# Kernel optimization log

Measured on AMD Instinct MI355X. Metric: run time of the kernel, lower is better.

The kernel has to match this reference:

```python
import jax, jax.numpy as jnp
import numpy as np

EPS = 1e-5

def layer_norm(x, gamma, beta):
    mu = jnp.mean(x, axis=-1, keepdims=True)
    var = jnp.mean(jnp.square(x - mu), axis=-1, keepdims=True)
    return (x - mu) * jax.lax.rsqrt(var + EPS) * gamma + beta

def setup_inputs() -> dict:
    key = jax.random.key(0)
    ks = jax.random.split(key, 8)
    B, N, E, D, H = 8, 10000, 160000, 128, 128  # batch, nodes, edges, in_dim, dim_h
    nodes = jax.random.normal(ks[0], (B, N, D), dtype=jnp.float32)
    senders = jax.random.randint(ks[1], (E,), 0, N)
    receivers = jax.random.randint(ks[2], (E,), 0, N)
    # nn.Linear(2*in_dim, in_dim): weight [out, in], bias [out]
    Wm = jax.random.normal(ks[3], (D, 2 * D), dtype=jnp.float32) / np.sqrt(2 * D)
    bm = jnp.zeros((D,), dtype=jnp.float32)
    # nn.Linear(2*in_dim, dim_h)
    Wn = jax.random.normal(ks[4], (H, 2 * D), dtype=jnp.float32) / np.sqrt(2 * D)
    bn = jnp.zeros((H,), dtype=jnp.float32)
    g1 = jnp.ones((D,), dtype=jnp.float32)
    b1 = jnp.zeros((D,), dtype=jnp.float32)
    g2 = jnp.ones((H,), dtype=jnp.float32)
    b2 = jnp.zeros((H,), dtype=jnp.float32)
    return {"nodes": nodes, "Wm": Wm, "bm": bm, "g1": g1, "b1": b1,
            "Wn": Wn, "bn": bn, "g2": g2, "b2": b2,
            "senders": senders, "receivers": receivers}

def reference(nodes, Wm, bm, g1, b1, Wn, bn, g2, b2, senders, receivers):
    # gather endpoints: [B, E, 2*D]
    edge_in = jnp.concatenate((nodes[:, receivers], nodes[:, senders]), axis=-1)
    messages = jnp.einsum('bed,od->beo', edge_in, Wm) + bm      # [B, E, D]
    messages = layer_norm(messages, g1, b1)
    # scatter-add into inbox along node axis
    inbox = jnp.zeros_like(nodes).at[:, receivers].add(messages)  # [B, N, D]
    node_in = jnp.concatenate((nodes, inbox), axis=-1)           # [B, N, 2*D]
    out = jnp.einsum('bnd,od->bno', node_in, Wn) + bn            # [B, N, H]
    return layer_norm(out, g2, b2)
```

## Files before the change

kernel.cpp:

```cpp
#include <hip/hip_runtime.h>

#define N_NODES 10000
#define N_EDGES 160000
#define BATCH   8
#define D       128
#define TWO_D   256
#define EPS     1e-5f
#define ETILE   32
#define TPB_E   8
#define TPB_N   8

typedef _Float16 f16x8  __attribute__((ext_vector_type(8)));
typedef float    f32x16 __attribute__((ext_vector_type(16)));

__global__ void zero_kernel(float4* __restrict__ p, long long n4) {
    long long idx    = (long long)blockIdx.x * blockDim.x + threadIdx.x;
    long long stride = (long long)gridDim.x * blockDim.x;
    const float4 z = {0.f, 0.f, 0.f, 0.f};
    for (long long i = idx; i < n4; i += stride) p[i] = z;
}

__global__ void prep_w(const float* __restrict__ Wm, const float* __restrict__ Wn,
                       unsigned char* __restrict__ img) {
    int t = blockIdx.x * blockDim.x + threadIdx.x;
    if (t >= 4096) return;
    int g = t >> 7, o = t & 127;
    f16x8 vm, vn;
#pragma unroll
    for (int j = 0; j < 8; ++j) {
        vm[j] = (_Float16)Wm[o * TWO_D + 8 * g + j];
        vn[j] = (_Float16)Wn[o * TWO_D + 8 * g + j];
    }
    ((f16x8*)img)[t]           = vm;
    ((f16x8*)(img + 65536))[t] = vn;
}

__global__ void hist_kernel(const int* __restrict__ recv, int* __restrict__ counts) {
    int e = blockIdx.x * blockDim.x + threadIdx.x;
    if (e < N_EDGES) atomicAdd(&counts[recv[e]], 1);
}

__global__ __launch_bounds__(1024)
void scan_kernel(const int* __restrict__ counts, int* __restrict__ cursor) {
    __shared__ int tmp[1024];
    int t = threadIdx.x;
    int local[10];
    int s = 0;
#pragma unroll
    for (int j = 0; j < 10; ++j) {
        int idx = t * 10 + j;
        int v = (idx < N_NODES) ? counts[idx] : 0;
        local[j] = s; s += v;
    }
    tmp[t] = s; __syncthreads();
    for (int off = 1; off < 1024; off <<= 1) {
        int v = tmp[t];
        int add = (t >= off) ? tmp[t - off] : 0;
        __syncthreads();
        tmp[t] = v + add;
        __syncthreads();
    }
    int base = (t > 0) ? tmp[t - 1] : 0;
#pragma unroll
    for (int j = 0; j < 10; ++j) {
        int idx = t * 10 + j;
        if (idx < N_NODES) cursor[idx] = base + local[j];
    }
}

__global__ void scatter_kernel(const int* __restrict__ recv, int* __restrict__ cursor,
                               int* __restrict__ perm) {
    int e = blockIdx.x * blockDim.x + threadIdx.x;
    if (e < N_EDGES) {
        int p = atomicAdd(&cursor[recv[e]], 1);
        perm[p] = e;
    }
}

__global__ __launch_bounds__(256, 2)
void edge_mfma(const float* __restrict__ nodes,
               const unsigned char* __restrict__ wimg,
               const float* __restrict__ bm,
               const float* __restrict__ g1,
               const float* __restrict__ b1,
               const int*   __restrict__ senders,
               const int*   __restrict__ receivers,
               const int*   __restrict__ perm,
               float* __restrict__ inbox) {
    __shared__ __align__(16) unsigned char s_lds[33280];
    __shared__ int   s_recv[ETILE];
    __shared__ float s_mu[ETILE];
    __shared__ float s_rs[ETILE];

    const int tid    = threadIdx.x;
    const int b      = blockIdx.y;
    const int w      = tid >> 6;
    const int l      = tid & 63;
    const int lane31 = l & 31;
    const int hiG    = l >> 5;
    const int o      = w * 32 + lane31;

    f16x8 wf[16];
    {
        const f16x8* img = (const f16x8*)wimg;
#pragma unroll
        for (int ks = 0; ks < 16; ++ks)
            wf[ks] = img[(2 * ks + hiG) * 128 + o];
    }
    const float bmv = bm[o];
    const int   col  = tid & 127;
    const int   half = tid >> 7;
    const float gv = g1[col], bv = b1[col];
    float* const abase = inbox + (size_t)b * N_NODES * D + col;

    const int i  = tid & 31;
    const int q8 = tid >> 5;
    f16x8* const Xh  = (f16x8*)s_lds;
    f16x8* const Xl  = (f16x8*)(s_lds + 16384);
    float* const msg = (float*)(s_lds + 16384);

    for (int it = 0; it < TPB_E; ++it) {
        const int e0 = (blockIdx.x * TPB_E + it) * ETILE;

        {
            const int pe = perm[e0 + i];
            const int r  = (q8 < 4) ? receivers[pe] : senders[pe];
            if (q8 == 0) s_recv[i] = r;
            const float* row = nodes + ((size_t)b * N_NODES + r) * D + (q8 & 3) * 32;
#pragma unroll
            for (int j = 0; j < 4; ++j) {
                const float4 va = *(const float4*)(row + 8 * j);
                const float4 vb = *(const float4*)(row + 8 * j + 4);
                const float xs[8] = {va.x, va.y, va.z, va.w, vb.x, vb.y, vb.z, vb.w};
                f16x8 h, lo;
#pragma unroll
                for (int u = 0; u < 8; ++u) {
                    h[u]  = (_Float16)xs[u];
                    lo[u] = (_Float16)(xs[u] - (float)h[u]);
                }
                const int g = 4 * q8 + j;
                Xh[g * 32 + i] = h;
                Xl[g * 32 + i] = lo;
            }
        }
        __syncthreads();

        f32x16 acc;
#pragma unroll
        for (int r = 0; r < 16; ++r) acc[r] = 0.f;
#pragma unroll
        for (int ks = 0; ks < 16; ++ks) {
            const f16x8 ah = Xh[(2 * ks + hiG) * 32 + lane31];
            const f16x8 al = Xl[(2 * ks + hiG) * 32 + lane31];
            acc = __builtin_amdgcn_mfma_f32_32x32x16_f16(ah, wf[ks], acc, 0, 0, 0);
            acc = __builtin_amdgcn_mfma_f32_32x32x16_f16(al, wf[ks], acc, 0, 0, 0);
        }
        __syncthreads();

#pragma unroll
        for (int r = 0; r < 16; ++r) {
            const int m = (r & 3) + 8 * (r >> 2) + 4 * hiG;
            msg[m * 132 + o] = acc[r] + bmv;
        }
        __syncthreads();

        {
            const int m = tid >> 3, c0 = tid & 7;
            float s = 0.f, s2 = 0.f;
#pragma unroll
            for (int i2 = 0; i2 < 16; ++i2) {
                const float v = msg[m * 132 + c0 + 8 * i2];
                s += v; s2 += v * v;
            }
            s  += __shfl_xor(s, 1, 64);  s  += __shfl_xor(s, 2, 64);  s  += __shfl_xor(s, 4, 64);
            s2 += __shfl_xor(s2, 1, 64); s2 += __shfl_xor(s2, 2, 64); s2 += __shfl_xor(s2, 4, 64);
            if (c0 == 0) {
                const float mu  = s * (1.f / 128.f);
                const float var = s2 * (1.f / 128.f) - mu * mu;
                s_mu[m] = mu;
                s_rs[m] = rsqrtf(var + EPS);
            }
        }
        __syncthreads();

        {
            int prev = -1; float accu = 0.f;
#pragma unroll
            for (int e = 0; e < 16; ++e) {
                const int ee = half * 16 + e;
                const int r  = s_recv[ee];
                const float val = (msg[ee * 132 + col] - s_mu[ee]) * s_rs[ee] * gv + bv;
                if (r != prev) {
                    if (prev >= 0) atomicAdd(abase + (size_t)prev * D, accu);
                    prev = r; accu = val;
                } else {
                    accu += val;
                }
            }
            if (prev >= 0) atomicAdd(abase + (size_t)prev * D, accu);
        }
        __syncthreads();
    }
}

__global__ __launch_bounds__(256, 2)
void node_mfma(const float* __restrict__ nodes,
               const float* __restrict__ inbox,
               const unsigned char* __restrict__ wimg,
               const float* __restrict__ bn,
               const float* __restrict__ g2,
               const float* __restrict__ b2,
               float* __restrict__ out) {
    __shared__ __align__(16) unsigned char s_lds[33280];
    __shared__ float s_mu[ETILE];
    __shared__ float s_rs[ETILE];

    const int tid    = threadIdx.x;
    const int b      = blockIdx.y;
    const int w      = tid >> 6;
    const int l      = tid & 63;
    const int lane31 = l & 31;
    const int hiG    = l >> 5;
    const int o      = w * 32 + lane31;

    f16x8 wf[16];
    {
        const f16x8* img = (const f16x8*)wimg;
#pragma unroll
        for (int ks = 0; ks < 16; ++ks)
            wf[ks] = img[(2 * ks + hiG) * 128 + o];
    }
    const float bnv = bn[o];
    const int   col  = tid & 127;
    const int   half = tid >> 7;
    const float gv = g2[col], bv = b2[col];

    const int i  = tid & 31;
    const int q8 = tid >> 5;
    f16x8* const Xh  = (f16x8*)s_lds;
    f16x8* const Xl  = (f16x8*)(s_lds + 16384);
    float* const msg = (float*)(s_lds + 16384);

    const int NTILES = (N_NODES + ETILE - 1) / ETILE;

    for (int it = 0; it < TPB_N; ++it) {
        const int tile = blockIdx.x * TPB_N + it;
        if (tile >= NTILES) break;
        const int n0 = tile * ETILE;

        {
            int n = n0 + i;
            if (n >= N_NODES) n = N_NODES - 1;
            const float* row = (q8 < 4)
                ? (nodes + ((size_t)b * N_NODES + n) * D + (q8 & 3) * 32)
                : (inbox + ((size_t)b * N_NODES + n) * D + (q8 & 3) * 32);
#pragma unroll
            for (int j = 0; j < 4; ++j) {
                const float4 va = *(const float4*)(row + 8 * j);
                const float4 vb = *(const float4*)(row + 8 * j + 4);
                const float xs[8] = {va.x, va.y, va.z, va.w, vb.x, vb.y, vb.z, vb.w};
                f16x8 h, lo;
#pragma unroll
                for (int u = 0; u < 8; ++u) {
                    h[u]  = (_Float16)xs[u];
                    lo[u] = (_Float16)(xs[u] - (float)h[u]);
                }
                const int g = 4 * q8 + j;
                Xh[g * 32 + i] = h;
                Xl[g * 32 + i] = lo;
            }
        }
        __syncthreads();

        f32x16 acc;
#pragma unroll
        for (int r = 0; r < 16; ++r) acc[r] = 0.f;
#pragma unroll
        for (int ks = 0; ks < 16; ++ks) {
            const f16x8 ah = Xh[(2 * ks + hiG) * 32 + lane31];
            const f16x8 al = Xl[(2 * ks + hiG) * 32 + lane31];
            acc = __builtin_amdgcn_mfma_f32_32x32x16_f16(ah, wf[ks], acc, 0, 0, 0);
            acc = __builtin_amdgcn_mfma_f32_32x32x16_f16(al, wf[ks], acc, 0, 0, 0);
        }
        __syncthreads();

#pragma unroll
        for (int r = 0; r < 16; ++r) {
            const int m = (r & 3) + 8 * (r >> 2) + 4 * hiG;
            msg[m * 132 + o] = acc[r] + bnv;
        }
        __syncthreads();

        {
            const int m = tid >> 3, c0 = tid & 7;
            float s = 0.f, s2 = 0.f;
#pragma unroll
            for (int i2 = 0; i2 < 16; ++i2) {
                const float v = msg[m * 132 + c0 + 8 * i2];
                s += v; s2 += v * v;
            }
            s  += __shfl_xor(s, 1, 64);  s  += __shfl_xor(s, 2, 64);  s  += __shfl_xor(s, 4, 64);
            s2 += __shfl_xor(s2, 1, 64); s2 += __shfl_xor(s2, 2, 64); s2 += __shfl_xor(s2, 4, 64);
            if (c0 == 0) {
                const float mu  = s * (1.f / 128.f);
                const float var = s2 * (1.f / 128.f) - mu * mu;
                s_mu[m] = mu;
                s_rs[m] = rsqrtf(var + EPS);
            }
        }
        __syncthreads();

        {
#pragma unroll
            for (int e = 0; e < 16; ++e) {
                const int ee = half * 16 + e;
                const int n  = n0 + ee;
                if (n < N_NODES) {
                    out[((size_t)b * N_NODES + n) * D + col] =
                        (msg[ee * 132 + col] - s_mu[ee]) * s_rs[ee] * gv + bv;
                }
            }
        }
        __syncthreads();
    }
}

__global__ __launch_bounds__(256, 2)
void edge_kernel(const float* __restrict__ nodes,
                 const float* __restrict__ Wm,
                 const float* __restrict__ bm,
                 const float* __restrict__ g1,
                 const float* __restrict__ b1,
                 const int*   __restrict__ senders,
                 const int*   __restrict__ receivers,
                 float* __restrict__ inbox) {
    __shared__ __align__(16) float ldsE[TWO_D][36];
    __shared__ __align__(16) float ldsW[64 * D];
    const int tid = threadIdx.x;
    const int b   = blockIdx.y;
    const int e0  = blockIdx.x * 32;
    const float* nb = nodes + (size_t)b * N_NODES * D;
    {
        const int i = tid >> 3, q0 = tid & 7, e = e0 + i;
        const float* rowR = nb + (size_t)receivers[e] * D;
        const float* rowS = nb + (size_t)senders[e] * D;
#pragma unroll
        for (int j = 0; j < 8; ++j) {
            const int k = (j * 8 + q0) * 4;
            const float4 v = (k < D) ? *(const float4*)(rowR + k)
                                     : *(const float4*)(rowS + (k - D));
            ldsE[k + 0][i] = v.x; ldsE[k + 1][i] = v.y;
            ldsE[k + 2][i] = v.z; ldsE[k + 3][i] = v.w;
        }
    }
    float acc[4][4];
#pragma unroll
    for (int a = 0; a < 4; ++a)
#pragma unroll
        for (int c = 0; c < 4; ++c) acc[a][c] = 0.0f;
    const int og = tid & 31, eg = tid >> 5;
    for (int kt = 0; kt < 4; ++kt) {
        __syncthreads();
        {
            const int oo = tid >> 1, half = tid & 1;
            const float* wrow = Wm + oo * TWO_D + kt * 64 + half * 32;
#pragma unroll
            for (int j = 0; j < 8; ++j) {
                const float4 w4 = *(const float4*)(wrow + j * 4);
                const int k2 = half * 32 + j * 4;
                ldsW[(k2 + 0) * D + oo] = w4.x; ldsW[(k2 + 1) * D + oo] = w4.y;
                ldsW[(k2 + 2) * D + oo] = w4.z; ldsW[(k2 + 3) * D + oo] = w4.w;
            }
        }
        __syncthreads();
#pragma unroll 4
        for (int k2 = 0; k2 < 64; ++k2) {
            const float4 wv = *(const float4*)&ldsW[k2 * D + 4 * og];
            const float4 xv = *(const float4*)&ldsE[kt * 64 + k2][4 * eg];
            const float wa[4] = {wv.x, wv.y, wv.z, wv.w};
            const float xa[4] = {xv.x, xv.y, xv.z, xv.w};
#pragma unroll
            for (int a = 0; a < 4; ++a)
#pragma unroll
                for (int c = 0; c < 4; ++c)
                    acc[a][c] = fmaf(xa[a], wa[c], acc[a][c]);
        }
    }
    const float4 bmv = *(const float4*)&bm[4 * og];
    const float4 g1v = *(const float4*)&g1[4 * og];
    const float4 b1v = *(const float4*)&b1[4 * og];
#pragma unroll
    for (int a = 0; a < 4; ++a) {
        acc[a][0] += bmv.x; acc[a][1] += bmv.y;
        acc[a][2] += bmv.z; acc[a][3] += bmv.w;
    }
    float mu[4], rs[4];
#pragma unroll
    for (int a = 0; a < 4; ++a) {
        float s = acc[a][0] + acc[a][1] + acc[a][2] + acc[a][3];
#pragma unroll
        for (int m = 16; m >= 1; m >>= 1) s += __shfl_xor(s, m, 64);
        mu[a] = s * (1.0f / 128.0f);
        const float d0 = acc[a][0] - mu[a], d1 = acc[a][1] - mu[a];
        const float d2 = acc[a][2] - mu[a], d3 = acc[a][3] - mu[a];
        float q = d0 * d0 + d1 * d1 + d2 * d2 + d3 * d3;
#pragma unroll
        for (int m = 16; m >= 1; m >>= 1) q += __shfl_xor(q, m, 64);
        rs[a] = rsqrtf(q * (1.0f / 128.0f) + EPS);
    }
#pragma unroll
    for (int a = 0; a < 4; ++a) {
        const int e = e0 + 4 * eg + a;
        const int r = receivers[e];
        float* dst = inbox + ((size_t)b * N_NODES + r) * D + 4 * og;
        atomicAdd(dst + 0, (acc[a][0] - mu[a]) * rs[a] * g1v.x + b1v.x);
        atomicAdd(dst + 1, (acc[a][1] - mu[a]) * rs[a] * g1v.y + b1v.y);
        atomicAdd(dst + 2, (acc[a][2] - mu[a]) * rs[a] * g1v.z + b1v.z);
        atomicAdd(dst + 3, (acc[a][3] - mu[a]) * rs[a] * g1v.w + b1v.w);
    }
}

__global__ __launch_bounds__(256, 2)
void node_kernel(const float* __restrict__ nodes,
                 const float* __restrict__ inbox,
                 const float* __restrict__ Wn,
                 const float* __restrict__ bn,
                 const float* __restrict__ g2,
                 const float* __restrict__ b2,
                 float* __restrict__ out) {
    __shared__ __align__(16) float ldsE[TWO_D][36];
    __shared__ __align__(16) float ldsW[64 * D];
    const int tid = threadIdx.x;
    const int b   = blockIdx.y;
    const int n0  = blockIdx.x * 32;
    {
        const int i = tid >> 3, q0 = tid & 7;
        int n = n0 + i;
        if (n >= N_NODES) n = N_NODES - 1;
        const float* rowN = nodes + ((size_t)b * N_NODES + n) * D;
        const float* rowI = inbox + ((size_t)b * N_NODES + n) * D;
#pragma unroll
        for (int j = 0; j < 8; ++j) {
            const int k = (j * 8 + q0) * 4;
            const float4 v = (k < D) ? *(const float4*)(rowN + k)
                                     : *(const float4*)(rowI + (k - D));
            ldsE[k + 0][i] = v.x; ldsE[k + 1][i] = v.y;
            ldsE[k + 2][i] = v.z; ldsE[k + 3][i] = v.w;
        }
    }
    float acc[4][4];
#pragma unroll
    for (int a = 0; a < 4; ++a)
#pragma unroll
        for (int c = 0; c < 4; ++c) acc[a][c] = 0.0f;
    const int og = tid & 31, eg = tid >> 5;
    for (int kt = 0; kt < 4; ++kt) {
        __syncthreads();
        {
            const int oo = tid >> 1, half = tid & 1;
            const float* wrow = Wn + oo * TWO_D + kt * 64 + half * 32;
#pragma unroll
            for (int j = 0; j < 8; ++j) {
                const float4 w4 = *(const float4*)(wrow + j * 4);
                const int k2 = half * 32 + j * 4;
                ldsW[(k2 + 0) * D + oo] = w4.x; ldsW[(k2 + 1) * D + oo] = w4.y;
                ldsW[(k2 + 2) * D + oo] = w4.z; ldsW[(k2 + 3) * D + oo] = w4.w;
            }
        }
        __syncthreads();
#pragma unroll 4
        for (int k2 = 0; k2 < 64; ++k2) {
            const float4 wv = *(const float4*)&ldsW[k2 * D + 4 * og];
            const float4 xv = *(const float4*)&ldsE[kt * 64 + k2][4 * eg];
            const float wa[4] = {wv.x, wv.y, wv.z, wv.w};
            const float xa[4] = {xv.x, xv.y, xv.z, xv.w};
#pragma unroll
            for (int a = 0; a < 4; ++a)
#pragma unroll
                for (int c = 0; c < 4; ++c)
                    acc[a][c] = fmaf(xa[a], wa[c], acc[a][c]);
        }
    }
    const float4 bnv = *(const float4*)&bn[4 * og];
    const float4 g2v = *(const float4*)&g2[4 * og];
    const float4 b2v = *(const float4*)&b2[4 * og];
#pragma unroll
    for (int a = 0; a < 4; ++a) {
        acc[a][0] += bnv.x; acc[a][1] += bnv.y;
        acc[a][2] += bnv.z; acc[a][3] += bnv.w;
    }
    float mu[4], rs[4];
#pragma unroll
    for (int a = 0; a < 4; ++a) {
        float s = acc[a][0] + acc[a][1] + acc[a][2] + acc[a][3];
#pragma unroll
        for (int m = 16; m >= 1; m >>= 1) s += __shfl_xor(s, m, 64);
        mu[a] = s * (1.0f / 128.0f);
        const float d0 = acc[a][0] - mu[a], d1 = acc[a][1] - mu[a];
        const float d2 = acc[a][2] - mu[a], d3 = acc[a][3] - mu[a];
        float q = d0 * d0 + d1 * d1 + d2 * d2 + d3 * d3;
#pragma unroll
        for (int m = 16; m >= 1; m >>= 1) q += __shfl_xor(q, m, 64);
        rs[a] = rsqrtf(q * (1.0f / 128.0f) + EPS);
    }
#pragma unroll
    for (int a = 0; a < 4; ++a) {
        const int n = n0 + 4 * eg + a;
        if (n < N_NODES) {
            float4 o4;
            o4.x = (acc[a][0] - mu[a]) * rs[a] * g2v.x + b2v.x;
            o4.y = (acc[a][1] - mu[a]) * rs[a] * g2v.y + b2v.y;
            o4.z = (acc[a][2] - mu[a]) * rs[a] * g2v.z + b2v.z;
            o4.w = (acc[a][3] - mu[a]) * rs[a] * g2v.w + b2v.w;
            *(float4*)(out + ((size_t)b * N_NODES + n) * D + 4 * og) = o4;
        }
    }
}

extern "C" void kernel_launch(void* const* d_in, const int* in_sizes, int n_in,
                              void* d_out, int out_size, void* d_ws, size_t ws_size,
                              hipStream_t stream) {
    const float* nodes     = (const float*)d_in[0];
    const float* Wm        = (const float*)d_in[1];
    const float* bm        = (const float*)d_in[2];
    const float* g1        = (const float*)d_in[3];
    const float* b1        = (const float*)d_in[4];
    const float* Wn        = (const float*)d_in[5];
    const float* bn        = (const float*)d_in[6];
    const float* g2        = (const float*)d_in[7];
    const float* b2        = (const float*)d_in[8];
    const int*   senders   = (const int*)d_in[9];
    const int*   receivers = (const int*)d_in[10];
    float*       out       = (float*)d_out;

    const long long inbox_n = (long long)BATCH * N_NODES * D;
    const size_t SCRATCH_NEED = 131072 + 720128;

    if (d_ws != nullptr && ws_size >= SCRATCH_NEED) {
        unsigned char* wsb  = (unsigned char*)d_ws;
        unsigned char* wimg = wsb;
        int* ints   = (int*)(wsb + 131072);
        int* counts = ints;
        int* cursor = ints + 10016;
        int* perm   = ints + 20032;
        float* inbox = (ws_size >= (size_t)1048576 + (size_t)inbox_n * 4)
                           ? (float*)(wsb + 1048576) : out;

        zero_kernel<<<dim3(10),   dim3(256), 0, stream>>>((float4*)counts, 2500);
        zero_kernel<<<dim3(2048), dim3(256), 0, stream>>>((float4*)inbox, inbox_n / 4);
        prep_w<<<dim3(16), dim3(256), 0, stream>>>(Wm, Wn, wimg);
        hist_kernel<<<dim3(625), dim3(256), 0, stream>>>(receivers, counts);
        scan_kernel<<<dim3(1), dim3(1024), 0, stream>>>(counts, cursor);
        scatter_kernel<<<dim3(625), dim3(256), 0, stream>>>(receivers, cursor, perm);

        edge_mfma<<<dim3(N_EDGES / ETILE / TPB_E, BATCH), dim3(256), 0, stream>>>(
            nodes, wimg, bm, g1, b1, senders, receivers, perm, inbox);

        const int ntiles = (N_NODES + ETILE - 1) / ETILE;
        node_mfma<<<dim3((ntiles + TPB_N - 1) / TPB_N, BATCH), dim3(256), 0, stream>>>(
            nodes, inbox, wimg + 65536, bn, g2, b2, out);
    } else {
        float* inbox = out;
        zero_kernel<<<dim3(2048), dim3(256), 0, stream>>>((float4*)inbox, inbox_n / 4);
        edge_kernel<<<dim3(N_EDGES / 32, BATCH), dim3(256), 0, stream>>>(
            nodes, Wm, bm, g1, b1, senders, receivers, inbox);
        node_kernel<<<dim3((N_NODES + 31) / 32, BATCH), dim3(256), 0, stream>>>(
            nodes, inbox, Wn, bn, g2, b2, out);
    }
}
```

Baseline: 460.9 us.

## Raise occupancy and interleave batches in block index for edge and node kernels

```diff
diff --git a/kernel.cpp b/kernel.cpp
--- a/kernel.cpp
+++ b/kernel.cpp
@@ -12,6 +12,7 @@
 
 typedef _Float16 f16x8  __attribute__((ext_vector_type(8)));
 typedef float    f32x16 __attribute__((ext_vector_type(16)));
+typedef int      intx4  __attribute__((ext_vector_type(4)));
 
 __global__ void zero_kernel(float4* __restrict__ p, long long n4) {
     long long idx    = (long long)blockIdx.x * blockDim.x + threadIdx.x;
@@ -77,7 +78,7 @@
     }
 }
 
-__global__ __launch_bounds__(256, 2)
+__global__ __launch_bounds__(256, 4)
 void edge_mfma(const float* __restrict__ nodes,
                const unsigned char* __restrict__ wimg,
                const float* __restrict__ bm,
@@ -93,19 +94,23 @@
     __shared__ float s_rs[ETILE];
 
     const int tid    = threadIdx.x;
-    const int b      = blockIdx.y;
+    const int b      = blockIdx.x & 7;
+    const int grp    = blockIdx.x >> 3;
     const int w      = tid >> 6;
     const int l      = tid & 63;
     const int lane31 = l & 31;
     const int hiG    = l >> 5;
     const int o      = w * 32 + lane31;
 
-    f16x8 wf[16];
+    intx4 wfi[16];
     {
-        const f16x8* img = (const f16x8*)wimg;
+        const intx4* img = (const intx4*)wimg;
 #pragma unroll
         for (int ks = 0; ks < 16; ++ks)
-            wf[ks] = img[(2 * ks + hiG) * 128 + o];
+            wfi[ks] = img[(2 * ks + hiG) * 128 + o];
+#pragma unroll
+        for (int ks = 0; ks < 16; ++ks)
+            asm volatile("" : "+v"(wfi[ks]));
     }
     const float bmv = bm[o];
     const int   col  = tid & 127;
@@ -120,7 +125,7 @@
     float* const msg = (float*)(s_lds + 16384);
 
     for (int it = 0; it < TPB_E; ++it) {
-        const int e0 = (blockIdx.x * TPB_E + it) * ETILE;
+        const int e0 = (grp * TPB_E + it) * ETILE;
 
         {
             const int pe = perm[e0 + i];
@@ -152,8 +157,9 @@
         for (int ks = 0; ks < 16; ++ks) {
             const f16x8 ah = Xh[(2 * ks + hiG) * 32 + lane31];
             const f16x8 al = Xl[(2 * ks + hiG) * 32 + lane31];
-            acc = __builtin_amdgcn_mfma_f32_32x32x16_f16(ah, wf[ks], acc, 0, 0, 0);
-            acc = __builtin_amdgcn_mfma_f32_32x32x16_f16(al, wf[ks], acc, 0, 0, 0);
+            const f16x8 wk = __builtin_bit_cast(f16x8, wfi[ks]);
+            acc = __builtin_amdgcn_mfma_f32_32x32x16_f16(ah, wk, acc, 0, 0, 0);
+            acc = __builtin_amdgcn_mfma_f32_32x32x16_f16(al, wk, acc, 0, 0, 0);
         }
         __syncthreads();
 
@@ -203,7 +209,7 @@
     }
 }
 
-__global__ __launch_bounds__(256, 2)
+__global__ __launch_bounds__(256, 4)
 void node_mfma(const float* __restrict__ nodes,
                const float* __restrict__ inbox,
                const unsigned char* __restrict__ wimg,
@@ -216,19 +222,23 @@
     __shared__ float s_rs[ETILE];
 
     const int tid    = threadIdx.x;
-    const int b      = blockIdx.y;
+    const int b      = blockIdx.x & 7;
+    const int grp    = blockIdx.x >> 3;
     const int w      = tid >> 6;
     const int l      = tid & 63;
     const int lane31 = l & 31;
     const int hiG    = l >> 5;
     const int o      = w * 32 + lane31;
 
-    f16x8 wf[16];
+    intx4 wfi[16];
     {
-        const f16x8* img = (const f16x8*)wimg;
+        const intx4* img = (const intx4*)wimg;
 #pragma unroll
         for (int ks = 0; ks < 16; ++ks)
-            wf[ks] = img[(2 * ks + hiG) * 128 + o];
+            wfi[ks] = img[(2 * ks + hiG) * 128 + o];
+#pragma unroll
+        for (int ks = 0; ks < 16; ++ks)
+            asm volatile("" : "+v"(wfi[ks]));
     }
     const float bnv = bn[o];
     const int   col  = tid & 127;
@@ -244,7 +254,7 @@
     const int NTILES = (N_NODES + ETILE - 1) / ETILE;
 
     for (int it = 0; it < TPB_N; ++it) {
-        const int tile = blockIdx.x * TPB_N + it;
+        const int tile = grp * TPB_N + it;
         if (tile >= NTILES) break;
         const int n0 = tile * ETILE;
 
@@ -279,8 +289,9 @@
         for (int ks = 0; ks < 16; ++ks) {
             const f16x8 ah = Xh[(2 * ks + hiG) * 32 + lane31];
             const f16x8 al = Xl[(2 * ks + hiG) * 32 + lane31];
-            acc = __builtin_amdgcn_mfma_f32_32x32x16_f16(ah, wf[ks], acc, 0, 0, 0);
-            acc = __builtin_amdgcn_mfma_f32_32x32x16_f16(al, wf[ks], acc, 0, 0, 0);
+            const f16x8 wk = __builtin_bit_cast(f16x8, wfi[ks]);
+            acc = __builtin_amdgcn_mfma_f32_32x32x16_f16(ah, wk, acc, 0, 0, 0);
+            acc = __builtin_amdgcn_mfma_f32_32x32x16_f16(al, wk, acc, 0, 0, 0);
         }
         __syncthreads();
 
@@ -553,11 +564,11 @@
         scan_kernel<<<dim3(1), dim3(1024), 0, stream>>>(counts, cursor);
         scatter_kernel<<<dim3(625), dim3(256), 0, stream>>>(receivers, cursor, perm);
 
-        edge_mfma<<<dim3(N_EDGES / ETILE / TPB_E, BATCH), dim3(256), 0, stream>>>(
+        edge_mfma<<<dim3(N_EDGES / ETILE / TPB_E * BATCH), dim3(256), 0, stream>>>(
             nodes, wimg, bm, g1, b1, senders, receivers, perm, inbox);
 
         const int ntiles = (N_NODES + ETILE - 1) / ETILE;
-        node_mfma<<<dim3((ntiles + TPB_N - 1) / TPB_N, BATCH), dim3(256), 0, stream>>>(
+        node_mfma<<<dim3((ntiles + TPB_N - 1) / TPB_N * BATCH), dim3(256), 0, stream>>>(
             nodes, inbox, wimg + 65536, bn, g2, b2, out);
     } else {
         float* inbox = out;
```

After: 422.0 us. 8.5% less time.
